# Optimization experiments

Measured on AMD Instinct MI355X. Metric: run time of the kernel, lower is better.

The kernel has to match this reference:

```python
import jax, jax.numpy as jnp
import numpy as np

N, E = 50000, 800000
IN_DIM, HID, H, L = 256, 128, 4, 2
HD = HID // H
EPS = 1e-5


def _bn(x, g, b):
    # training-mode BatchNorm1d: biased variance over batch dim, eps=1e-5
    m = x.mean(0)
    v = jnp.var(x, axis=0)
    return g * (x - m) * jax.lax.rsqrt(v + EPS) + b


def _seg_softmax(scores, dst, n):
    # scores: [E, H]; softmax over edges sharing the same dst node
    m = jax.ops.segment_max(scores, dst, num_segments=n)  # [N, H]
    e = jnp.exp(scores - m[dst])
    s = jax.ops.segment_sum(e, dst, num_segments=n)
    return e / s[dst]


def _attn_layer(h, src, dst, wq, bq, wk, bk, wv, bv, wo, bo):
    n = h.shape[0]
    scale = 1.0 / np.sqrt(HD)
    Q = (h @ wq + bq).reshape(n, H, HD)
    K = (h @ wk + bk).reshape(n, H, HD)
    V = (h @ wv + bv).reshape(n, H, HD)
    # per-edge scores: Q of src dotted with K of dst
    scores = jnp.einsum('ehd,ehd->eh', Q[src], K[dst]) * scale  # [E, H]
    attn = _seg_softmax(scores, dst, n)                         # [E, H]
    # weighted scatter-sum of V gathered at dst (faithful to source)
    out = jax.ops.segment_sum(attn[:, :, None] * V[dst], dst, num_segments=n)
    out = out.reshape(n, HID) @ wo + bo
    return jax.nn.relu(out)


def setup_inputs() -> dict:
    key = jax.random.key(0)
    ks = jax.random.split(key, 20)
    s = 0.05  # weight scale to keep activations tame
    inp = {
        'x': jax.random.normal(ks[0], (N, IN_DIM), jnp.float32),
        'edge_index': jax.random.randint(ks[1], (2, E), 0, N),
        'W_enc1': jax.random.normal(ks[2], (IN_DIM, HID), jnp.float32) * s,
        'b_enc1': jax.random.normal(ks[3], (HID,), jnp.float32) * s,
        'g1': jnp.ones((HID,), jnp.float32),
        'beta1': jnp.zeros((HID,), jnp.float32),
        'W_enc2': jax.random.normal(ks[4], (HID, HID), jnp.float32) * s,
        'b_enc2': jax.random.normal(ks[5], (HID,), jnp.float32) * s,
        'g2': jnp.ones((HID,), jnp.float32),
        'beta2': jnp.zeros((HID,), jnp.float32),
        'Wq': jax.random.normal(ks[6], (L, HID, HID), jnp.float32) * s,
        'bq': jax.random.normal(ks[7], (L, HID), jnp.float32) * s,
        'Wk': jax.random.normal(ks[8], (L, HID, HID), jnp.float32) * s,
        'bk': jax.random.normal(ks[9], (L, HID), jnp.float32) * s,
        'Wv': jax.random.normal(ks[10], (L, HID, HID), jnp.float32) * s,
        'bv': jax.random.normal(ks[11], (L, HID), jnp.float32) * s,
        'Wo': jax.random.normal(ks[12], (L, HID, HID), jnp.float32) * s,
        'bo': jax.random.normal(ks[13], (L, HID), jnp.float32) * s,
    }
    return inp


def reference(x, edge_index, W_enc1, b_enc1, g1, beta1, W_enc2, b_enc2, g2, beta2,
              Wq, bq, Wk, bk, Wv, bv, Wo, bo):
    src, dst = edge_index[0], edge_index[1]
    # encoder: Linear -> BN -> ReLU -> (dropout=id) -> Linear -> BN -> ReLU
    h = jax.nn.relu(_bn(x @ W_enc1 + b_enc1, g1, beta1))
    h = jax.nn.relu(_bn(h @ W_enc2 + b_enc2, g2, beta2))
    for i in range(L):
        h = _attn_layer(h, src, dst, Wq[i], bq[i], Wk[i], bk[i],
                        Wv[i], bv[i], Wo[i], bo[i])
    return h
```

## Files before the change

### kernel.cpp

```cpp
#include <hip/hip_runtime.h>

#define NN 50000
#define NE 800000
#define NB 1563
#define NBM 3125
#define TOTF 114688

typedef unsigned short u16;
typedef unsigned int u32;
typedef __attribute__((ext_vector_type(8))) short s8v;
typedef __attribute__((ext_vector_type(4))) float f4v;

__device__ __forceinline__ void split2(float f, u16& h, u16& lo) {
    u32 u = __float_as_uint(f);
    h = (u16)(u >> 16);
    float r = f - __uint_as_float(u & 0xFFFF0000u);
    lo = (u16)(__float_as_uint(r) >> 16);
}

__global__ void prep_k(float* __restrict__ mask,
                       const float* __restrict__ W1, const float* __restrict__ W2,
                       const float* __restrict__ Wv, const float* __restrict__ Wo,
                       u16* __restrict__ fh, u16* __restrict__ fl) {
    int i = blockIdx.x * 256 + threadIdx.x;
    if (i < NN) mask[i] = 0.f;
    if (i < TOTF) {
        const float* W;
        int local;
        if (i < 32768) { W = W1; local = i; }
        else {
            int t = i - 32768;
            int m = t >> 14;
            local = t & 16383;
            if (m == 0) W = W2;
            else if (m == 1) W = Wv;
            else if (m == 2) W = Wo;
            else if (m == 3) W = Wv + 16384;
            else W = Wo + 16384;
        }
        int j = local & 7, l = (local >> 3) & 63, nt = (local >> 9) & 7, kc = local >> 12;
        int k = kc * 32 + ((l >> 4) << 3) + j;
        int n = nt * 16 + (l & 15);
        u16 h, lo;
        split2(W[k * 128 + n], h, lo);
        fh[i] = h;
        fl[i] = lo;
    }
}

__global__ __launch_bounds__(64)
void redstats_k(const float* __restrict__ pst, float* __restrict__ st) {
    int c = blockIdx.x;
    float s = 0.f;
    for (int b = threadIdx.x; b < NB; b += 64) s += pst[(size_t)c * NB + b];
    s += __shfl_xor(s, 1);  s += __shfl_xor(s, 2);  s += __shfl_xor(s, 4);
    s += __shfl_xor(s, 8);  s += __shfl_xor(s, 16); s += __shfl_xor(s, 32);
    if (threadIdx.x == 0) st[c] = s;
}

template<int KC, int FOLD, int STATS, int SCAT>
__global__ __launch_bounds__(256, 8)
void mgemm_k(const float* __restrict__ A,
             const u16* __restrict__ fh, const u16* __restrict__ fl,
             const float* __restrict__ bias,
             const float* __restrict__ fst,
             const float* __restrict__ fg, const float* __restrict__ fbe,
             const int* __restrict__ dstv,
             float* __restrict__ maskw,
             float* __restrict__ pst,
             float* __restrict__ C) {
    constexpr int KP = KC / 4;
    __shared__ __align__(16) u16 Ah[32][136];
    __shared__ __align__(16) u16 Al[32][136];
    __shared__ float scl[128], shf[128];
    const int tid = threadIdx.x;
    const int l = tid & 63, w = tid >> 6;
    const int q = l >> 4, cc = l & 15;
    const int sl = w >> 1, hf = w & 1;
    const int row0 = blockIdx.x * 32;

    if (SCAT) {
        int e2 = (blockIdx.x * 256 + tid) * 2;
        if (e2 + 1 < NE) {
            int2 dd = *(const int2*)(dstv + e2);
            maskw[dd.x] = 1.0f;
            maskw[dd.y] = 1.0f;
        }
    }

    if (FOLD && tid < 128) {
        float mean = fst[tid] * (1.0f / NN);
        float var = fst[128 + tid] * (1.0f / NN) - mean * mean;
        float rstd = rsqrtf(var + 1e-5f);
        float ga = fg[tid] * rstd;
        scl[tid] = ga;
        shf[tid] = fbe[tid] - mean * ga;
    }

    f4v zf = {0.f, 0.f, 0.f, 0.f};
    f4v acc[4];
#pragma unroll
    for (int t = 0; t < 4; ++t) acc[t] = zf;

    float4 pref[4];
#pragma unroll
    for (int it = 0; it < 4; ++it) {
        int lin = tid + 256 * it;
        int r = lin >> 5;
        int c4 = (lin & 31) * 4;
        int gr = row0 + r; if (gr > NN - 1) gr = NN - 1;
        pref[it] = *(const float4*)(A + (size_t)gr * (KC * 32) + c4);
    }

    for (int p = 0; p < KP; ++p) {
        if (p > 0 || FOLD) __syncthreads();
#pragma unroll
        for (int it = 0; it < 4; ++it) {
            int lin = tid + 256 * it;
            int r = lin >> 5;
            int c4 = (lin & 31) * 4;
            float v[4] = {pref[it].x, pref[it].y, pref[it].z, pref[it].w};
            if (FOLD) {
#pragma unroll
                for (int m = 0; m < 4; ++m) {
                    float t = v[m] * scl[c4 + m] + shf[c4 + m];
                    v[m] = t > 0.f ? t : 0.f;
                }
            }
            ushort4 uh, ul;
            split2(v[0], uh.x, ul.x); split2(v[1], uh.y, ul.y);
            split2(v[2], uh.z, ul.z); split2(v[3], uh.w, ul.w);
            *(ushort4*)&Ah[r][c4] = uh;
            *(ushort4*)&Al[r][c4] = ul;
        }
        __syncthreads();
        if (p + 1 < KP) {
#pragma unroll
            for (int it = 0; it < 4; ++it) {
                int lin = tid + 256 * it;
                int r = lin >> 5;
                int c4 = (lin & 31) * 4;
                int gr = row0 + r; if (gr > NN - 1) gr = NN - 1;
                pref[it] = *(const float4*)(A + (size_t)gr * (KC * 32) + (p + 1) * 128 + c4);
            }
        }
#pragma unroll
        for (int kc = 0; kc < 4; ++kc) {
            int kcg = p * 4 + kc;
            s8v ah = *(const s8v*)&Ah[16 * sl + cc][kc * 32 + q * 8];
            s8v al = *(const s8v*)&Al[16 * sl + cc][kc * 32 + q * 8];
#pragma unroll
            for (int t = 0; t < 4; ++t) {
                const int fo = kcg * 4096 + (4 * hf + t) * 512 + l * 8;
                s8v bh = *(const s8v*)(fh + fo);
                s8v bl = *(const s8v*)(fl + fo);
                acc[t] = __builtin_amdgcn_mfma_f32_16x16x32_bf16(ah, bh, acc[t], 0, 0, 0);
                acc[t] = __builtin_amdgcn_mfma_f32_16x16x32_bf16(ah, bl, acc[t], 0, 0, 0);
                acc[t] = __builtin_amdgcn_mfma_f32_16x16x32_bf16(al, bh, acc[t], 0, 0, 0);
            }
        }
    }

    float ps[4], pq[4];
#pragma unroll
    for (int t = 0; t < 4; ++t) { ps[t] = 0.f; pq[t] = 0.f; }
#pragma unroll
    for (int t = 0; t < 4; ++t) {
        int col = (4 * hf + t) * 16 + cc;
        float bb = bias[col];
#pragma unroll
        for (int r = 0; r < 4; ++r) {
            int gr = row0 + 16 * sl + q * 4 + r;
            float val = acc[t][r] + bb;
            if (gr < NN) {
                C[(size_t)gr * 128 + col] = val;
                if (STATS) { ps[t] += val; pq[t] += val * val; }
            }
        }
    }
    if (STATS) {
        __syncthreads();
        float* wredS = (float*)&Ah[0][0];
        float* wredQ = wredS + 256;
#pragma unroll
        for (int t = 0; t < 4; ++t) {
            ps[t] += __shfl_xor(ps[t], 16); ps[t] += __shfl_xor(ps[t], 32);
            pq[t] += __shfl_xor(pq[t], 16); pq[t] += __shfl_xor(pq[t], 32);
        }
        if (l < 16) {
#pragma unroll
            for (int t = 0; t < 4; ++t) {
                int col = (4 * hf + t) * 16 + l;
                wredS[sl * 128 + col] = ps[t];
                wredQ[sl * 128 + col] = pq[t];
            }
        }
        __syncthreads();
        int c = tid & 127;
        const float* src = (tid < 128) ? wredS : wredQ;
        pst[(size_t)tid * NB + blockIdx.x] = src[c] + src[128 + c];
    }
}

__global__ __launch_bounds__(128, 8)
void mmega_k(const float* __restrict__ X,
             const u16* __restrict__ fh, const u16* __restrict__ fl,
             const float* __restrict__ bv, const float* __restrict__ bo,
             const float* __restrict__ fst,
             const float* __restrict__ fg, const float* __restrict__ fbe,
             const float* __restrict__ mask, float* __restrict__ out) {
    __shared__ __align__(16) u16 Ah[16][136];
    __shared__ __align__(16) u16 Al[16][136];
    __shared__ float scl[128], shf[128];
    const int tid = threadIdx.x;
    const int l = tid & 63, w = tid >> 6;
    const int q = l >> 4, cc = l & 15;
    const int hf = w;
    const int row0 = blockIdx.x * 16;

    if (tid < 128) {
        float mean = fst[tid] * (1.0f / NN);
        float var = fst[128 + tid] * (1.0f / NN) - mean * mean;
        float rstd = rsqrtf(var + 1e-5f);
        float ga = fg[tid] * rstd;
        scl[tid] = ga;
        shf[tid] = fbe[tid] - mean * ga;
    }
    __syncthreads();

    float rm[4];
#pragma unroll
    for (int r = 0; r < 4; ++r) {
        int gr = row0 + q * 4 + r;
        rm[r] = (gr < NN) ? mask[gr] : 0.f;
    }

#pragma unroll
    for (int it = 0; it < 4; ++it) {
        int lin = tid + 128 * it;
        int r = lin >> 5;
        int c4 = (lin & 31) * 4;
        int gr = row0 + r; if (gr > NN - 1) gr = NN - 1;
        float4 f = *(const float4*)(X + (size_t)gr * 128 + c4);
        float v[4] = {f.x, f.y, f.z, f.w};
        ushort4 uh, ul;
#pragma unroll
        for (int m = 0; m < 4; ++m) {
            float t = v[m] * scl[c4 + m] + shf[c4 + m];
            v[m] = t > 0.f ? t : 0.f;
        }
        split2(v[0], uh.x, ul.x); split2(v[1], uh.y, ul.y);
        split2(v[2], uh.z, ul.z); split2(v[3], uh.w, ul.w);
        *(ushort4*)&Ah[r][c4] = uh;
        *(ushort4*)&Al[r][c4] = ul;
    }
    __syncthreads();

    f4v zf = {0.f, 0.f, 0.f, 0.f};
    for (int s = 0; s < 4; ++s) {
        const u16* WH = fh + s * 16384;
        const u16* WL = fl + s * 16384;
        const float* bp = (s == 0) ? bv : (s == 1) ? bo : (s == 2) ? (bv + 128) : (bo + 128);

        f4v acc[4];
#pragma unroll
        for (int t = 0; t < 4; ++t) acc[t] = zf;
#pragma unroll
        for (int kc = 0; kc < 4; ++kc) {
            s8v ah = *(const s8v*)&Ah[cc][kc * 32 + q * 8];
            s8v al = *(const s8v*)&Al[cc][kc * 32 + q * 8];
#pragma unroll
            for (int t = 0; t < 4; ++t) {
                const int fo = kc * 4096 + (4 * hf + t) * 512 + l * 8;
                s8v bh = *(const s8v*)(WH + fo);
                s8v bl = *(const s8v*)(WL + fo);
                acc[t] = __builtin_amdgcn_mfma_f32_16x16x32_bf16(ah, bh, acc[t], 0, 0, 0);
                acc[t] = __builtin_amdgcn_mfma_f32_16x16x32_bf16(ah, bl, acc[t], 0, 0, 0);
                acc[t] = __builtin_amdgcn_mfma_f32_16x16x32_bf16(al, bh, acc[t], 0, 0, 0);
            }
        }

        if (s == 3) {
#pragma unroll
            for (int t = 0; t < 4; ++t) {
                int col = (4 * hf + t) * 16 + cc;
                float bb = bp[col];
#pragma unroll
                for (int r = 0; r < 4; ++r) {
                    int gr = row0 + q * 4 + r;
                    if (gr < NN)
                        out[(size_t)gr * 128 + col] = fmaxf(acc[t][r] + bb, 0.f);
                }
            }
        } else {
            __syncthreads();
#pragma unroll
            for (int t = 0; t < 4; ++t) {
                int col = (4 * hf + t) * 16 + cc;
                float bb = bp[col];
#pragma unroll
                for (int r = 0; r < 4; ++r) {
                    int rl = q * 4 + r;
                    float val = acc[t][r] + bb;
                    val = (s == 1) ? fmaxf(val, 0.f) : val * rm[r];
                    u16 h, lo; split2(val, h, lo);
                    Ah[rl][col] = h;
                    Al[rl][col] = lo;
                }
            }
            __syncthreads();
        }
    }
}

extern "C" void kernel_launch(void* const* d_in, const int* in_sizes, int n_in,
                              void* d_out, int out_size, void* d_ws, size_t ws_size,
                              hipStream_t stream) {
    const float* x   = (const float*)d_in[0];
    const int*   ei  = (const int*)d_in[1];
    const float* W1  = (const float*)d_in[2];
    const float* b1  = (const float*)d_in[3];
    const float* g1  = (const float*)d_in[4];
    const float* be1 = (const float*)d_in[5];
    const float* W2  = (const float*)d_in[6];
    const float* b2  = (const float*)d_in[7];
    const float* g2  = (const float*)d_in[8];
    const float* be2 = (const float*)d_in[9];
    const float* Wv  = (const float*)d_in[14];
    const float* bv  = (const float*)d_in[15];
    const float* Wo  = (const float*)d_in[16];
    const float* bo  = (const float*)d_in[17];

    float* out = (float*)d_out;

    char* ws = (char*)d_ws;
    float* buf  = (float*)(ws);
    float* mask = (float*)(ws + 25600000);
    float* st1  = (float*)(ws + 25800704);
    float* st2  = st1 + 256;
    u16*   fH   = (u16*)(ws + 25804800);
    u16*   fL   = fH + TOTF;
    float* pst  = (float*)(ws + 26263552);

    prep_k<<<dim3((TOTF + 255) / 256), dim3(256), 0, stream>>>(
        mask, W1, W2, Wv, Wo, fH, fL);

    dim3 gg(NB), bb(256);
    mgemm_k<8, 0, 1, 1><<<gg, bb, 0, stream>>>(x, fH, fL, b1,
                                               nullptr, nullptr, nullptr,
                                               ei + NE, mask, pst, buf);
    redstats_k<<<dim3(256), dim3(64), 0, stream>>>(pst, st1);
    mgemm_k<4, 1, 1, 0><<<gg, bb, 0, stream>>>(buf, fH + 32768, fL + 32768, b2,
                                               st1, g1, be1,
                                               nullptr, nullptr, pst, out);
    redstats_k<<<dim3(256), dim3(64), 0, stream>>>(pst, st2);
    mmega_k<<<dim3(NBM), dim3(128), 0, stream>>>(out, fH + 49152, fL + 49152, bv, bo,
                                                 st2, g2, be2, mask, out);
}
```

Baseline: 221.3 us.

## Give each wave a private 16-row tile over all 128 columns, dropping block barriers

Both GEMM kernels are restructured so each of two waves in a 128-thread block owns its own 16-row slab and computes all 8 column tiles, with its own LDS staging buffer. This removes most __syncthreads, the shared-memory BN scale/shift tables (now computed per thread in registers), and the cross-wave register prefetch pipeline. The edge mask scatter becomes a grid-stride loop. The trade is more accumulator registers per wave (8 f4v tiles), lower declared occupancy, and loss of the global-load prefetch overlap.

```diff
diff --git a/kernel.cpp b/kernel.cpp
--- a/kernel.cpp
+++ b/kernel.cpp
@@ -3,7 +3,6 @@
 #define NN 50000
 #define NE 800000
 #define NB 1563
-#define NBM 3125
 #define TOTF 114688
 
 typedef unsigned short u16;
@@ -59,7 +58,7 @@
 }
 
 template<int KC, int FOLD, int STATS, int SCAT>
-__global__ __launch_bounds__(256, 8)
+__global__ __launch_bounds__(128, 4)
 void mgemm_k(const float* __restrict__ A,
              const u16* __restrict__ fh, const u16* __restrict__ fl,
              const float* __restrict__ bias,
@@ -70,88 +69,65 @@
              float* __restrict__ pst,
              float* __restrict__ C) {
     constexpr int KP = KC / 4;
-    __shared__ __align__(16) u16 Ah[32][136];
-    __shared__ __align__(16) u16 Al[32][136];
-    __shared__ float scl[128], shf[128];
+    __shared__ __align__(16) u16 Ah[2][16][136];
+    __shared__ __align__(16) u16 Al[2][16][136];
     const int tid = threadIdx.x;
     const int l = tid & 63, w = tid >> 6;
     const int q = l >> 4, cc = l & 15;
-    const int sl = w >> 1, hf = w & 1;
-    const int row0 = blockIdx.x * 32;
+    const int wrow0 = blockIdx.x * 32 + w * 16;
+    const int c0 = (l & 31) * 4;
 
     if (SCAT) {
-        int e2 = (blockIdx.x * 256 + tid) * 2;
-        if (e2 + 1 < NE) {
-            int2 dd = *(const int2*)(dstv + e2);
-            maskw[dd.x] = 1.0f;
-            maskw[dd.y] = 1.0f;
-        }
-    }
-
-    if (FOLD && tid < 128) {
-        float mean = fst[tid] * (1.0f / NN);
-        float var = fst[128 + tid] * (1.0f / NN) - mean * mean;
-        float rstd = rsqrtf(var + 1e-5f);
-        float ga = fg[tid] * rstd;
-        scl[tid] = ga;
-        shf[tid] = fbe[tid] - mean * ga;
+        for (int e = blockIdx.x * 128 + tid; e < NE; e += NB * 128)
+            maskw[dstv[e]] = 1.0f;
+    }
+
+    float ga[4], sh[4];
+    if (FOLD) {
+#pragma unroll
+        for (int m = 0; m < 4; ++m) {
+            int c = c0 + m;
+            float mean = fst[c] * (1.0f / NN);
+            float var = fst[128 + c] * (1.0f / NN) - mean * mean;
+            float gi = fg[c] * rsqrtf(var + 1e-5f);
+            ga[m] = gi;
+            sh[m] = fbe[c] - mean * gi;
+        }
     }
 
     f4v zf = {0.f, 0.f, 0.f, 0.f};
-    f4v acc[4];
-#pragma unroll
-    for (int t = 0; t < 4; ++t) acc[t] = zf;
-
-    float4 pref[4];
-#pragma unroll
-    for (int it = 0; it < 4; ++it) {
-        int lin = tid + 256 * it;
-        int r = lin >> 5;
-        int c4 = (lin & 31) * 4;
-        int gr = row0 + r; if (gr > NN - 1) gr = NN - 1;
-        pref[it] = *(const float4*)(A + (size_t)gr * (KC * 32) + c4);
-    }
+    f4v acc[8];
+#pragma unroll
+    for (int t = 0; t < 8; ++t) acc[t] = zf;
 
     for (int p = 0; p < KP; ++p) {
-        if (p > 0 || FOLD) __syncthreads();
-#pragma unroll
-        for (int it = 0; it < 4; ++it) {
-            int lin = tid + 256 * it;
-            int r = lin >> 5;
-            int c4 = (lin & 31) * 4;
-            float v[4] = {pref[it].x, pref[it].y, pref[it].z, pref[it].w};
+#pragma unroll
+        for (int it = 0; it < 8; ++it) {
+            int r = (l >> 5) + 2 * it;
+            int gr = wrow0 + r; if (gr > NN - 1) gr = NN - 1;
+            float4 f = *(const float4*)(A + (size_t)gr * (KC * 32) + p * 128 + c0);
+            float v[4] = {f.x, f.y, f.z, f.w};
             if (FOLD) {
 #pragma unroll
                 for (int m = 0; m < 4; ++m) {
-                    float t = v[m] * scl[c4 + m] + shf[c4 + m];
+                    float t = v[m] * ga[m] + sh[m];
                     v[m] = t > 0.f ? t : 0.f;
                 }
             }
             ushort4 uh, ul;
             split2(v[0], uh.x, ul.x); split2(v[1], uh.y, ul.y);
             split2(v[2], uh.z, ul.z); split2(v[3], uh.w, ul.w);
-            *(ushort4*)&Ah[r][c4] = uh;
-            *(ushort4*)&Al[r][c4] = ul;
-        }
-        __syncthreads();
-        if (p + 1 < KP) {
-#pragma unroll
-            for (int it = 0; it < 4; ++it) {
-                int lin = tid + 256 * it;
-                int r = lin >> 5;
-                int c4 = (lin & 31) * 4;
-                int gr = row0 + r; if (gr > NN - 1) gr = NN - 1;
-                pref[it] = *(const float4*)(A + (size_t)gr * (KC * 32) + (p + 1) * 128 + c4);
-            }
+            *(ushort4*)&Ah[w][r][c0] = uh;
+            *(ushort4*)&Al[w][r][c0] = ul;
         }
 #pragma unroll
         for (int kc = 0; kc < 4; ++kc) {
             int kcg = p * 4 + kc;
-            s8v ah = *(const s8v*)&Ah[16 * sl + cc][kc * 32 + q * 8];
-            s8v al = *(const s8v*)&Al[16 * sl + cc][kc * 32 + q * 8];
-#pragma unroll
-            for (int t = 0; t < 4; ++t) {
-                const int fo = kcg * 4096 + (4 * hf + t) * 512 + l * 8;
+            s8v ah = *(const s8v*)&Ah[w][cc][kc * 32 + q * 8];
+            s8v al = *(const s8v*)&Al[w][cc][kc * 32 + q * 8];
+#pragma unroll
+            for (int t = 0; t < 8; ++t) {
+                const int fo = kcg * 4096 + t * 512 + l * 8;
                 s8v bh = *(const s8v*)(fh + fo);
                 s8v bl = *(const s8v*)(fl + fo);
                 acc[t] = __builtin_amdgcn_mfma_f32_16x16x32_bf16(ah, bh, acc[t], 0, 0, 0);
@@ -161,16 +137,16 @@
         }
     }
 
-    float ps[4], pq[4];
-#pragma unroll
-    for (int t = 0; t < 4; ++t) { ps[t] = 0.f; pq[t] = 0.f; }
-#pragma unroll
-    for (int t = 0; t < 4; ++t) {
-        int col = (4 * hf + t) * 16 + cc;
+    float ps[8], pq[8];
+#pragma unroll
+    for (int t = 0; t < 8; ++t) { ps[t] = 0.f; pq[t] = 0.f; }
+#pragma unroll
+    for (int t = 0; t < 8; ++t) {
+        int col = t * 16 + cc;
         float bb = bias[col];
 #pragma unroll
         for (int r = 0; r < 4; ++r) {
-            int gr = row0 + 16 * sl + q * 4 + r;
+            int gr = wrow0 + q * 4 + r;
             float val = acc[t][r] + bb;
             if (gr < NN) {
                 C[(size_t)gr * 128 + col] = val;
@@ -179,82 +155,80 @@
         }
     }
     if (STATS) {
-        __syncthreads();
-        float* wredS = (float*)&Ah[0][0];
-        float* wredQ = wredS + 256;
-#pragma unroll
-        for (int t = 0; t < 4; ++t) {
+#pragma unroll
+        for (int t = 0; t < 8; ++t) {
             ps[t] += __shfl_xor(ps[t], 16); ps[t] += __shfl_xor(ps[t], 32);
             pq[t] += __shfl_xor(pq[t], 16); pq[t] += __shfl_xor(pq[t], 32);
         }
+        __syncthreads();
+        float* wr = (float*)&Ah[0][0][0];
         if (l < 16) {
 #pragma unroll
-            for (int t = 0; t < 4; ++t) {
-                int col = (4 * hf + t) * 16 + l;
-                wredS[sl * 128 + col] = ps[t];
-                wredQ[sl * 128 + col] = pq[t];
+            for (int t = 0; t < 8; ++t) {
+                int col = t * 16 + l;
+                wr[w * 256 + col] = ps[t];
+                wr[w * 256 + 128 + col] = pq[t];
             }
         }
         __syncthreads();
-        int c = tid & 127;
-        const float* src = (tid < 128) ? wredS : wredQ;
-        pst[(size_t)tid * NB + blockIdx.x] = src[c] + src[128 + c];
-    }
-}
-
-__global__ __launch_bounds__(128, 8)
+        {
+            int c = tid;
+            pst[(size_t)c * NB + blockIdx.x]         = wr[c] + wr[256 + c];
+            pst[(size_t)(128 + c) * NB + blockIdx.x] = wr[128 + c] + wr[384 + c];
+        }
+    }
+}
+
+__global__ __launch_bounds__(128, 4)
 void mmega_k(const float* __restrict__ X,
              const u16* __restrict__ fh, const u16* __restrict__ fl,
              const float* __restrict__ bv, const float* __restrict__ bo,
              const float* __restrict__ fst,
              const float* __restrict__ fg, const float* __restrict__ fbe,
              const float* __restrict__ mask, float* __restrict__ out) {
-    __shared__ __align__(16) u16 Ah[16][136];
-    __shared__ __align__(16) u16 Al[16][136];
-    __shared__ float scl[128], shf[128];
+    __shared__ __align__(16) u16 Ah[2][16][136];
+    __shared__ __align__(16) u16 Al[2][16][136];
     const int tid = threadIdx.x;
     const int l = tid & 63, w = tid >> 6;
     const int q = l >> 4, cc = l & 15;
-    const int hf = w;
-    const int row0 = blockIdx.x * 16;
-
-    if (tid < 128) {
-        float mean = fst[tid] * (1.0f / NN);
-        float var = fst[128 + tid] * (1.0f / NN) - mean * mean;
-        float rstd = rsqrtf(var + 1e-5f);
-        float ga = fg[tid] * rstd;
-        scl[tid] = ga;
-        shf[tid] = fbe[tid] - mean * ga;
-    }
-    __syncthreads();
+    const int wrow0 = blockIdx.x * 32 + w * 16;
+    const int c0 = (l & 31) * 4;
+
+    float ga[4], sh[4];
+#pragma unroll
+    for (int m = 0; m < 4; ++m) {
+        int c = c0 + m;
+        float mean = fst[c] * (1.0f / NN);
+        float var = fst[128 + c] * (1.0f / NN) - mean * mean;
+        float gi = fg[c] * rsqrtf(var + 1e-5f);
+        ga[m] = gi;
+        sh[m] = fbe[c] - mean * gi;
+    }
 
     float rm[4];
 #pragma unroll
     for (int r = 0; r < 4; ++r) {
-        int gr = row0 + q * 4 + r;
+        int gr = wrow0 + q * 4 + r;
         rm[r] = (gr < NN) ? mask[gr] : 0.f;
     }
 
 #pragma unroll
-    for (int it = 0; it < 4; ++it) {
-        int lin = tid + 128 * it;
-        int r = lin >> 5;
-        int c4 = (lin & 31) * 4;
-        int gr = row0 + r; if (gr > NN - 1) gr = NN - 1;
-        float4 f = *(const float4*)(X + (size_t)gr * 128 + c4);
+    for (int it = 0; it < 8; ++it) {
+        int r = (l >> 5) + 2 * it;
+        int gr = wrow0 + r; if (gr > NN - 1) gr = NN - 1;
+        float4 f = *(const float4*)(X + (size_t)gr * 128 + c0);
         float v[4] = {f.x, f.y, f.z, f.w};
+#pragma unroll
+        for (int m = 0; m < 4; ++m) {
+            float t = v[m] * ga[m] + sh[m];
+            v[m] = t > 0.f ? t : 0.f;
+        }
         ushort4 uh, ul;
-#pragma unroll
-        for (int m = 0; m < 4; ++m) {
-            float t = v[m] * scl[c4 + m] + shf[c4 + m];
-            v[m] = t > 0.f ? t : 0.f;
-        }
         split2(v[0], uh.x, ul.x); split2(v[1], uh.y, ul.y);
         split2(v[2], uh.z, ul.z); split2(v[3], uh.w, ul.w);
-        *(ushort4*)&Ah[r][c4] = uh;
-        *(ushort4*)&Al[r][c4] = ul;
-    }
-    __syncthreads();
+        *(ushort4*)&Ah[w][r][c0] = uh;
+        *(ushort4*)&Al[w][r][c0] = ul;
+    }
 
     f4v zf = {0.f, 0.f, 0.f, 0.f};
     for (int s = 0; s < 4; ++s) {
@@ -262,16 +236,16 @@
         const u16* WL = fl + s * 16384;
         const float* bp = (s == 0) ? bv : (s == 1) ? bo : (s == 2) ? (bv + 128) : (bo + 128);
 
-        f4v acc[4];
-#pragma unroll
-        for (int t = 0; t < 4; ++t) acc[t] = zf;
+        f4v acc[8];
+#pragma unroll
+        for (int t = 0; t < 8; ++t) acc[t] = zf;
 #pragma unroll
         for (int kc = 0; kc < 4; ++kc) {
-            s8v ah = *(const s8v*)&Ah[cc][kc * 32 + q * 8];
-            s8v al = *(const s8v*)&Al[cc][kc * 32 + q * 8];
-#pragma unroll
-            for (int t = 0; t < 4; ++t) {
-                const int fo = kc * 4096 + (4 * hf + t) * 512 + l * 8;
+            s8v ah = *(const s8v*)&Ah[w][cc][kc * 32 + q * 8];
+            s8v al = *(const s8v*)&Al[w][cc][kc * 32 + q * 8];
+#pragma unroll
+            for (int t = 0; t < 8; ++t) {
+                const int fo = kc * 4096 + t * 512 + l * 8;
                 s8v bh = *(const s8v*)(WH + fo);
                 s8v bl = *(const s8v*)(WL + fo);
                 acc[t] = __builtin_amdgcn_mfma_f32_16x16x32_bf16(ah, bh, acc[t], 0, 0, 0);
@@ -282,21 +256,20 @@
 
         if (s == 3) {
 #pragma unroll
-            for (int t = 0; t < 4; ++t) {
-                int col = (4 * hf + t) * 16 + cc;
+            for (int t = 0; t < 8; ++t) {
+                int col = t * 16 + cc;
                 float bb = bp[col];
 #pragma unroll
                 for (int r = 0; r < 4; ++r) {
-                    int gr = row0 + q * 4 + r;
+                    int gr = wrow0 + q * 4 + r;
                     if (gr < NN)
                         out[(size_t)gr * 128 + col] = fmaxf(acc[t][r] + bb, 0.f);
                 }
             }
         } else {
-            __syncthreads();
-#pragma unroll
-            for (int t = 0; t < 4; ++t) {
-                int col = (4 * hf + t) * 16 + cc;
+#pragma unroll
+            for (int t = 0; t < 8; ++t) {
+                int col = t * 16 + cc;
                 float bb = bp[col];
 #pragma unroll
                 for (int r = 0; r < 4; ++r) {
@@ -304,11 +277,10 @@
                     float val = acc[t][r] + bb;
                     val = (s == 1) ? fmaxf(val, 0.f) : val * rm[r];
                     u16 h, lo; split2(val, h, lo);
-                    Ah[rl][col] = h;
-                    Al[rl][col] = lo;
+                    Ah[w][rl][col] = h;
+                    Al[w][rl][col] = lo;
                 }
             }
-            __syncthreads();
         }
     }
 }
@@ -345,7 +317,7 @@
     prep_k<<<dim3((TOTF + 255) / 256), dim3(256), 0, stream>>>(
         mask, W1, W2, Wv, Wo, fH, fL);
 
-    dim3 gg(NB), bb(256);
+    dim3 gg(NB), bb(128);
     mgemm_k<8, 0, 1, 1><<<gg, bb, 0, stream>>>(x, fH, fL, b1,
                                                nullptr, nullptr, nullptr,
                                                ei + NE, mask, pst, buf);
@@ -354,6 +326,6 @@
                                                st1, g1, be1,
                                                nullptr, nullptr, pst, out);
     redstats_k<<<dim3(256), dim3(64), 0, stream>>>(pst, st2);
-    mmega_k<<<dim3(NBM), dim3(128), 0, stream>>>(out, fH + 49152, fL + 49152, bv, bo,
-                                                 st2, g2, be2, mask, out);
-}
+    mmega_k<<<gg, bb, 0, stream>>>(out, fH + 49152, fL + 49152, bv, bo,
+                                   st2, g2, be2, mask, out);
+}
```

Measured after the change: 234.6 us. 6.0% more time.
